# Optimization experiments

Measured on AMD Instinct MI355X. Metric: run time of the kernel, lower is better.

Reference implementation:

```python
import jax, jax.numpy as jnp
import numpy as np
import math

HIDDEN = 768
HEADS = 12
HEAD_DIM = HIDDEN // HEADS
B, N = 128, 196
POS = 196


def setup_inputs() -> dict:
    key = jax.random.key(0)
    ks = jax.random.split(key, 12)
    s = 1.0 / math.sqrt(HIDDEN)
    inp = {
        "x": jax.random.normal(ks[0], (B, N, HIDDEN), dtype=jnp.float32),
        "Wq": jax.random.normal(ks[1], (HIDDEN, HIDDEN), dtype=jnp.float32) * s,
        "bq": jnp.zeros((HIDDEN,), dtype=jnp.float32),
        "Wk": jax.random.normal(ks[2], (HIDDEN, HIDDEN), dtype=jnp.float32) * s,
        "bk": jnp.zeros((HIDDEN,), dtype=jnp.float32),
        "Wv": jax.random.normal(ks[3], (HIDDEN, HIDDEN), dtype=jnp.float32) * s,
        "bv": jnp.zeros((HIDDEN,), dtype=jnp.float32),
        "Wp": jax.random.normal(ks[4], (HIDDEN, HIDDEN), dtype=jnp.float32) * s,
        "bp": jnp.zeros((HIDDEN,), dtype=jnp.float32),
        "pos_bias": jax.random.normal(ks[5], (POS, POS), dtype=jnp.float32) * 0.02,
        "mask": jnp.ones((B, 1, 1, N), dtype=jnp.int32),
    }
    return inp


def reference(x, Wq, bq, Wk, bk, Wv, bv, Wp, bp, pos_bias, mask):
    Bx, Nx, C = x.shape
    H, D = HEADS, HEAD_DIM
    # nn.Linear: y = x @ W.T + b
    q = (x @ Wq.T + bq).reshape(Bx, Nx, H, D).transpose(0, 2, 1, 3)  # [B,H,N,D]
    k = (x @ Wk.T + bk).reshape(Bx, Nx, H, D).transpose(0, 2, 1, 3)
    v = (x @ Wv.T + bv).reshape(Bx, Nx, H, D).transpose(0, 2, 1, 3)
    attn = jnp.einsum('bhnd,bhmd->bhnm', q, k) / math.sqrt(D)
    attn = attn + pos_bias[:Nx, :Nx][None, None, :, :]
    attn = jnp.where(mask == 0, -jnp.inf, attn)
    attn = jax.nn.softmax(attn, axis=-1)
    out = jnp.einsum('bhnm,bhmd->bhnd', attn, v)
    out = out.transpose(0, 2, 1, 3).reshape(Bx, Nx, C)
    return out @ Wp.T + bp
```

## Files before the change

### kernel.cpp

```cpp
#include <hip/hip_runtime.h>
#include <hip/hip_bf16.h>

#define HIDDEN 768
#define HEADS 12
#define HEAD_DIM 64
#define BATCH 128
#define SEQ 196
#define M_TOT (BATCH * SEQ)
#define QKV_N (3 * HIDDEN)

typedef __attribute__((ext_vector_type(8))) short bf16x8;
typedef __attribute__((ext_vector_type(8))) unsigned short u16x8;
typedef __attribute__((ext_vector_type(4))) float f32x4;

__device__ __forceinline__ unsigned short f2bf(float f) {
    unsigned int u = __builtin_bit_cast(unsigned int, f);
    unsigned int r = (u + 0x7fffu + ((u >> 16) & 1u)) >> 16;
    return (unsigned short)r;
}

__device__ __forceinline__ ushort4 cvt4(float4 v) {
    ushort4 o;
    o.x = f2bf(v.x); o.y = f2bf(v.y); o.z = f2bf(v.z); o.w = f2bf(v.w);
    return o;
}

__global__ __launch_bounds__(256) void prep_kernel(
    const float* __restrict__ x,
    const float* __restrict__ Wq, const float* __restrict__ Wk,
    const float* __restrict__ Wv, const float* __restrict__ Wp,
    const float* __restrict__ bq, const float* __restrict__ bk,
    const float* __restrict__ bv,
    unsigned short* __restrict__ xb, unsigned short* __restrict__ wqkv,
    unsigned short* __restrict__ wpb, float* __restrict__ biasq)
{
    const long long NX = (long long)M_TOT * HIDDEN / 4;
    const long long NQ = NX + (long long)QKV_N * HIDDEN / 4;
    const long long NP = NQ + (long long)HIDDEN * HIDDEN / 4;
    const long long NB = NP + QKV_N / 4;
    long long tid = (long long)blockIdx.x * 256 + threadIdx.x;
    if (tid < NX) {
        float4 v = ((const float4*)x)[tid];
        ((ushort4*)xb)[tid] = cvt4(v);
    } else if (tid < NQ) {
        int i = (int)(tid - NX);
        int e = i * 4;
        int row = e / HIDDEN, col = e % HIDDEN;
        const float* s = (row < HIDDEN) ? (Wq + (size_t)row * HIDDEN + col)
                       : (row < 2 * HIDDEN) ? (Wk + (size_t)(row - HIDDEN) * HIDDEN + col)
                       : (Wv + (size_t)(row - 2 * HIDDEN) * HIDDEN + col);
        ((ushort4*)wqkv)[i] = cvt4(*(const float4*)s);
    } else if (tid < NP) {
        int i = (int)(tid - NQ);
        ((ushort4*)wpb)[i] = cvt4(((const float4*)Wp)[i]);
    } else if (tid < NB) {
        int i = (int)(tid - NP);
        int e = i * 4;
        const float* s = (e < HIDDEN) ? (bq + e)
                       : (e < 2 * HIDDEN) ? (bk + (e - HIDDEN))
                       : (bv + (e - 2 * HIDDEN));
        *(float4*)(biasq + e) = *(const float4*)s;
    }
}

template <bool OUT_BF16>
__global__ __launch_bounds__(512, 2) void gemm256(
    const unsigned short* __restrict__ A,
    const unsigned short* __restrict__ B,
    const float* __restrict__ bias,
    void* __restrict__ C, const int Ncols)
{
    __shared__ __align__(16) unsigned short SMEM[65536];
    const int t = threadIdx.x, w = t >> 6, lane = t & 63;
    const int quad = lane >> 4, l15 = lane & 15;
    const int wm = w >> 2, wn = w & 3;

    const int gx = gridDim.x;
    const int nwg = gx * (int)gridDim.y;
    const int orig = blockIdx.y * gx + blockIdx.x;
    const int qq = nwg >> 3, rr = nwg & 7;
    const int xcd = orig & 7, loc = orig >> 3;
    const int wg = (xcd < rr ? xcd * (qq + 1) : rr * (qq + 1) + (xcd - rr) * qq) + loc;
    const int m0 = (wg / gx) * 256, n0 = (wg % gx) * 256;

    const int row64 = t >> 3, slot = t & 7;
    const int ksw = (slot ^ (row64 & 7)) << 3;
    const unsigned short* Ag = A + (size_t)m0 * HIDDEN + ksw;
    const unsigned short* Bg = B + (size_t)n0 * HIDDEN + ksw;
    const int ldsw = (w << 3) * 64;

#define STAGEA(bb, tt, pp)                                                          \
    __builtin_amdgcn_global_load_lds(                                               \
        (__attribute__((address_space(1))) void*)(Ag + (size_t)((pp) * 64 + row64) * HIDDEN + (tt) * 64), \
        (__attribute__((address_space(3))) void*)(SMEM + (bb) * 16384 + (pp) * 4096 + ldsw), 16, 0, 0)
#define STAGEB(bb, tt, pp)                                                          \
    __builtin_amdgcn_global_load_lds(                                               \
        (__attribute__((address_space(1))) void*)(Bg + (size_t)((pp) * 64 + row64) * HIDDEN + (tt) * 64), \
        (__attribute__((address_space(3))) void*)(SMEM + 32768 + (bb) * 16384 + (pp) * 4096 + ldsw), 16, 0, 0)

    const int sw = l15 & 7;
    const int s0 = (quad ^ sw) << 3;
    const int s1 = ((quad + 4) ^ sw) << 3;
    const unsigned short* pa = SMEM + (wm * 128 + l15) * 64;
    const unsigned short* pb = SMEM + 32768 + (wn * 64 + l15) * 64;

    f32x4 acc[8][4] = {};

#pragma unroll
    for (int p = 0; p < 4; ++p) STAGEA(0, 0, p);
#pragma unroll
    for (int p = 0; p < 4; ++p) STAGEB(0, 0, p);
#pragma unroll
    for (int p = 0; p < 4; ++p) STAGEB(1, 1, p);
    asm volatile("s_waitcnt vmcnt(4)" ::: "memory");
    __builtin_amdgcn_s_barrier();

#pragma unroll 2
    for (int kt = 0; kt < 12; ++kt) {
        const int b = kt & 1;
        const unsigned short* pab = pa + b * 16384;
        const unsigned short* pbb = pb + b * 16384;
        bf16x8 Bf[4][2];
        bf16x8 Af[2][2];

#pragma unroll
        for (int ph = 0; ph < 4; ++ph) {
            const int ib = ph * 2;
            if (ph == 0) {
#pragma unroll
                for (int j = 0; j < 4; ++j) {
                    Bf[j][0] = *(const bf16x8*)(pbb + j * 1024 + s0);
                    Bf[j][1] = *(const bf16x8*)(pbb + j * 1024 + s1);
                }
            }
            Af[0][0] = *(const bf16x8*)(pab + ib * 1024 + s0);
            Af[0][1] = *(const bf16x8*)(pab + ib * 1024 + s1);
            Af[1][0] = *(const bf16x8*)(pab + ib * 1024 + 1024 + s0);
            Af[1][1] = *(const bf16x8*)(pab + ib * 1024 + 1024 + s1);
            if (ph == 0 && kt < 11) { STAGEA(b ^ 1, kt + 1, 0); STAGEA(b ^ 1, kt + 1, 1); }
            if (ph == 1 && kt < 11) { STAGEA(b ^ 1, kt + 1, 2); STAGEA(b ^ 1, kt + 1, 3); }
            if (ph == 2 && kt < 10) { STAGEB(b, kt + 2, 0); STAGEB(b, kt + 2, 1); }
            if (ph == 3 && kt < 10) { STAGEB(b, kt + 2, 2); STAGEB(b, kt + 2, 3); }
            __builtin_amdgcn_s_barrier();
            asm volatile("s_waitcnt lgkmcnt(0)" ::: "memory");
            __builtin_amdgcn_sched_barrier(0);
            __builtin_amdgcn_s_setprio(1);
#pragma unroll
            for (int i = 0; i < 2; ++i)
#pragma unroll
                for (int j = 0; j < 4; ++j) {
                    acc[ib + i][j] = __builtin_amdgcn_mfma_f32_16x16x32_bf16(
                        Af[i][0], Bf[j][0], acc[ib + i][j], 0, 0, 0);
                    acc[ib + i][j] = __builtin_amdgcn_mfma_f32_16x16x32_bf16(
                        Af[i][1], Bf[j][1], acc[ib + i][j], 0, 0, 0);
                }
            __builtin_amdgcn_s_setprio(0);
            if (ph == 3) {
                if (kt < 10) { asm volatile("s_waitcnt vmcnt(4)" ::: "memory"); }
                else if (kt == 10) { asm volatile("s_waitcnt vmcnt(0)" ::: "memory"); }
            }
            __builtin_amdgcn_s_barrier();
        }
    }
#undef STAGEA
#undef STAGEB

    __syncthreads();
    float* Cs = (float*)SMEM + w * (16 * 68);
    float bvj[4];
#pragma unroll
    for (int j = 0; j < 4; ++j) bvj[j] = bias[n0 + wn * 64 + j * 16 + l15];

#pragma unroll
    for (int i = 0; i < 8; ++i) {
        __builtin_amdgcn_sched_barrier(0);
#pragma unroll
        for (int j = 0; j < 4; ++j)
#pragma unroll
            for (int r = 0; r < 4; ++r)
                Cs[(quad * 4 + r) * 68 + j * 16 + l15] = acc[i][j][r] + bvj[j];
        __builtin_amdgcn_sched_barrier(0);
        asm volatile("s_waitcnt lgkmcnt(0)" ::: "memory");
        if constexpr (OUT_BF16) {
#pragma unroll
            for (int p = 0; p < 2; ++p) {
                const int row = p * 8 + (lane >> 3);
                const int c0 = (lane & 7) * 8;
                float4 a = *(const float4*)&Cs[row * 68 + c0];
                float4 bb = *(const float4*)&Cs[row * 68 + c0 + 4];
                u16x8 pk;
                pk[0] = f2bf(a.x); pk[1] = f2bf(a.y); pk[2] = f2bf(a.z); pk[3] = f2bf(a.w);
                pk[4] = f2bf(bb.x); pk[5] = f2bf(bb.y); pk[6] = f2bf(bb.z); pk[7] = f2bf(bb.w);
                *(u16x8*)((unsigned short*)C +
                          (size_t)(m0 + wm * 128 + i * 16 + row) * Ncols + n0 + wn * 64 + c0) = pk;
            }
        } else {
#pragma unroll
            for (int p = 0; p < 4; ++p) {
                const int row = p * 4 + (lane >> 4);
                const int c0 = (lane & 15) * 4;
                float4 a = *(const float4*)&Cs[row * 68 + c0];
                *(float4*)((float*)C +
                           (size_t)(m0 + wm * 128 + i * 16 + row) * Ncols + n0 + wn * 64 + c0) = a;
            }
        }
        __builtin_amdgcn_sched_barrier(0);
    }
}

__global__ __launch_bounds__(256, 2) void attn_kernel(
    const unsigned short* __restrict__ QKV,
    const float* __restrict__ pos_bias,
    const int* __restrict__ mask,
    unsigned short* __restrict__ ctx)
{
    __shared__ __align__(16) unsigned short Ks[208 * 72];
    __shared__ __align__(16) unsigned short Vt[64 * 256];
    __shared__ __align__(16) unsigned short Os[4][16 * 72];
    const int b = blockIdx.x / HEADS, h = blockIdx.x % HEADS;
    const int t = threadIdx.x, w = t >> 6, lane = t & 63;
    const int quad = lane >> 4, l15 = lane & 15;
    const size_t base = (size_t)b * SEQ * QKV_N + h * HEAD_DIM;

    for (int c = t; c < SEQ * 8; c += 256) {
        int row = c >> 3, d0 = (c & 7) * 8;
        *(bf16x8*)(Ks + row * 72 + d0) =
            *(const bf16x8*)(QKV + base + (size_t)row * QKV_N + HIDDEN + d0);
    }
    {
        bf16x8 z = {};
        for (int i = t; i < 12 * 9; i += 256) {
            int row = 196 + i / 9, d0 = (i % 9) * 8;
            *(bf16x8*)(Ks + row * 72 + d0) = z;
        }
    }
    for (int i = t; i < 64 * 60; i += 256) {
        int row = i / 60, key = 196 + i % 60;
        int s = (row & 7) ^ ((row >> 3) & 7);
        Vt[row * 256 + ((((key >> 3) ^ s) << 3) | (key & 7))] = 0;
    }
    for (int c = t; c < SEQ * 8; c += 256) {
        int key = c >> 3, d0 = (c & 7) * 8;
        bf16x8 vv = *(const bf16x8*)(QKV + base + (size_t)key * QKV_N + 2 * HIDDEN + d0);
        int cb = key >> 3, kk = key & 7;
#pragma unroll
        for (int j = 0; j < 8; ++j) {
            int row = d0 + j;
            int s = (row & 7) ^ ((row >> 3) & 7);
            Vt[row * 256 + (((cb ^ s) << 3) | kk)] = (unsigned short)vv[j];
        }
    }
    __syncthreads();

    int vs[4];
#pragma unroll
    for (int nt = 0; nt < 4; ++nt) {
        int rr = nt * 16 + l15;
        vs[nt] = (rr & 7) ^ ((rr >> 3) & 7);
    }

    for (int t16 = w; t16 < 13; t16 += 4) {
        const int qrow = min(t16 * 16 + l15, SEQ - 1);
        const unsigned short* qp = QKV + base + (size_t)qrow * QKV_N + quad * 8;
        bf16x8 qf0 = *(const bf16x8*)(qp);
        bf16x8 qf1 = *(const bf16x8*)(qp + 32);

        f32x4 accT[13];
#pragma unroll
        for (int jt = 0; jt < 13; ++jt) {
            const unsigned short* kp = Ks + (jt * 16 + l15) * 72 + quad * 8;
            bf16x8 kf0 = *(const bf16x8*)(kp);
            bf16x8 kf1 = *(const bf16x8*)(kp + 32);
            f32x4 z = {};
            z = __builtin_amdgcn_mfma_f32_16x16x32_bf16(kf0, qf0, z, 0, 0, 0);
            z = __builtin_amdgcn_mfma_f32_16x16x32_bf16(kf1, qf1, z, 0, 0, 0);
            accT[jt] = z;
        }

        float mx = -3e38f;
#pragma unroll
        for (int jt = 0; jt < 13; ++jt) {
            const int key0 = jt * 16 + quad * 4;
            const int kb = min(key0, SEQ - 4);
            float4 pb = *(const float4*)(pos_bias + (size_t)qrow * SEQ + kb);
            int4 mk = *(const int4*)(mask + b * SEQ + kb);
#pragma unroll
            for (int r = 0; r < 4; ++r) {
                const int key = key0 + r;
                const bool cv = (key < SEQ) && ((&mk.x)[r] != 0);
                float v = cv ? (accT[jt][r] * 0.125f + (&pb.x)[r]) : -1e30f;
                accT[jt][r] = v;
                mx = fmaxf(mx, v);
            }
        }
        mx = fmaxf(mx, __shfl_xor(mx, 16, 64));
        mx = fmaxf(mx, __shfl_xor(mx, 32, 64));
        float sm = 0.f;
#pragma unroll
        for (int jt = 0; jt < 13; ++jt)
#pragma unroll
            for (int r = 0; r < 4; ++r) {
                float e = __expf(accT[jt][r] - mx);
                accT[jt][r] = e;
                sm += e;
            }
        sm += __shfl_xor(sm, 16, 64);
        sm += __shfl_xor(sm, 32, 64);
        const float inv = 1.0f / sm;

        unsigned int pk[14][2];
#pragma unroll
        for (int jt = 0; jt < 13; ++jt)
#pragma unroll
            for (int pp = 0; pp < 2; ++pp) {
                unsigned int lo = f2bf(accT[jt][2 * pp] * inv);
                unsigned int hi = f2bf(accT[jt][2 * pp + 1] * inv);
                pk[jt][pp] = (hi << 16) | lo;
            }
        pk[13][0] = 0; pk[13][1] = 0;

        f32x4 o[4] = {};
        const int hi_half = quad >> 1;
        const int sq0 = (quad & 1) * 2 * 16 + l15;
        const int sq1 = sq0 + 16;
#pragma unroll
        for (int kt = 0; kt < 7; ++kt) {
            union { unsigned int u[4]; bf16x8 v; } pf;
#pragma unroll
            for (int u = 0; u < 4; ++u) {
                const int src = (u < 2) ? sq0 : sq1;
                unsigned int a0 = (unsigned int)__shfl((int)pk[2 * kt][u & 1], src, 64);
                unsigned int a1 = (unsigned int)__shfl((int)pk[2 * kt + 1][u & 1], src, 64);
                pf.u[u] = hi_half ? a1 : a0;
            }
#pragma unroll
            for (int nt = 0; nt < 4; ++nt) {
                const int rr = nt * 16 + l15;
                const bf16x8 vf = *(const bf16x8*)(
                    &Vt[rr * 256 + (((kt * 4 + quad) ^ vs[nt]) << 3)]);
                o[nt] = __builtin_amdgcn_mfma_f32_16x16x32_bf16(pf.v, vf, o[nt], 0, 0, 0);
            }
        }

        __builtin_amdgcn_sched_barrier(0);
#pragma unroll
        for (int nt = 0; nt < 4; ++nt)
#pragma unroll
            for (int r = 0; r < 4; ++r)
                Os[w][(quad * 4 + r) * 72 + nt * 16 + l15] = f2bf(o[nt][r]);
        __builtin_amdgcn_sched_barrier(0);
        asm volatile("s_waitcnt lgkmcnt(0)" ::: "memory");
#pragma unroll
        for (int p = 0; p < 2; ++p) {
            const int row = p * 8 + (lane >> 3);
            const int grow = t16 * 16 + row;
            const int c0 = (lane & 7) * 8;
            bf16x8 ov = *(const bf16x8*)&Os[w][row * 72 + c0];
            if (grow < SEQ)
                *(bf16x8*)(ctx + ((size_t)b * SEQ + grow) * HIDDEN + h * HEAD_DIM + c0) = ov;
        }
        __builtin_amdgcn_sched_barrier(0);
    }
}

extern "C" void kernel_launch(void* const* d_in, const int* in_sizes, int n_in,
                              void* d_out, int out_size, void* d_ws, size_t ws_size,
                              hipStream_t stream) {
    const float* x    = (const float*)d_in[0];
    const float* Wq   = (const float*)d_in[1];
    const float* bq   = (const float*)d_in[2];
    const float* Wk   = (const float*)d_in[3];
    const float* bk   = (const float*)d_in[4];
    const float* Wv   = (const float*)d_in[5];
    const float* bv   = (const float*)d_in[6];
    const float* Wp   = (const float*)d_in[7];
    const float* bp   = (const float*)d_in[8];
    const float* pos  = (const float*)d_in[9];
    const int*   mask = (const int*)d_in[10];

    char* ws = (char*)d_ws;
    size_t off = 0;
    auto alloc = [&](size_t bytes) -> char* {
        char* p = ws + off;
        off += (bytes + 255) & ~(size_t)255;
        return p;
    };
    unsigned short* xb    = (unsigned short*)alloc((size_t)M_TOT * HIDDEN * 2);
    unsigned short* wqkv  = (unsigned short*)alloc((size_t)QKV_N * HIDDEN * 2);
    unsigned short* wpb   = (unsigned short*)alloc((size_t)HIDDEN * HIDDEN * 2);
    float*          biasq = (float*)alloc((size_t)QKV_N * 4);
    unsigned short* qkv   = (unsigned short*)alloc((size_t)M_TOT * QKV_N * 2);
    unsigned short* ctx   = (unsigned short*)alloc((size_t)M_TOT * HIDDEN * 2);

    prep_kernel<<<21123, 256, 0, stream>>>(x, Wq, Wk, Wv, Wp, bq, bk, bv,
                                           xb, wqkv, wpb, biasq);
    gemm256<true><<<dim3(QKV_N / 256, M_TOT / 256), 512, 0, stream>>>(
        xb, wqkv, biasq, (void*)qkv, QKV_N);
    attn_kernel<<<BATCH * HEADS, 256, 0, stream>>>(qkv, pos, mask, ctx);
    gemm256<false><<<dim3(HIDDEN / 256, M_TOT / 256), 512, 0, stream>>>(
        ctx, wpb, bp, d_out, HIDDEN);
}
```

Before: 377.2 us.

## Load B fragments directly from global into registers and quad-buffer A in LDS

The GEMM stops staging B tiles through LDS. Each wave now loads its B fragments straight from global memory into registers, one k-tile ahead, while A is staged in a 4-deep LDS ring with prefetch distance two. The workgroup-to-tile mapping becomes column-major so consecutive workgroups share the same B columns, which should improve L2 reuse. This removes LDS traffic and barriers for B and halves the per-phase barriers, but makes B loads uncached per-wave global reads and leaves MFMAs exposed to global latency if the prefetch is not deep enough.

```diff
diff --git a/kernel.cpp b/kernel.cpp
--- a/kernel.cpp
+++ b/kernel.cpp
@@ -75,95 +75,91 @@
     const int quad = lane >> 4, l15 = lane & 15;
     const int wm = w >> 2, wn = w & 3;
 
-    const int gx = gridDim.x;
-    const int nwg = gx * (int)gridDim.y;
-    const int orig = blockIdx.y * gx + blockIdx.x;
-    const int qq = nwg >> 3, rr = nwg & 7;
+    const int gy = gridDim.y;
+    const int nwg = gridDim.x * gy;
+    const int orig = blockIdx.y * gridDim.x + blockIdx.x;
+    const int qq = nwg >> 3, rr2 = nwg & 7;
     const int xcd = orig & 7, loc = orig >> 3;
-    const int wg = (xcd < rr ? xcd * (qq + 1) : rr * (qq + 1) + (xcd - rr) * qq) + loc;
-    const int m0 = (wg / gx) * 256, n0 = (wg % gx) * 256;
+    const int pos = (xcd < rr2 ? xcd * (qq + 1) : rr2 * (qq + 1) + (xcd - rr2) * qq) + loc;
+    const int m0 = (pos % gy) * 256;
+    const int n0 = (pos / gy) * 256;
 
     const int row64 = t >> 3, slot = t & 7;
     const int ksw = (slot ^ (row64 & 7)) << 3;
     const unsigned short* Ag = A + (size_t)m0 * HIDDEN + ksw;
-    const unsigned short* Bg = B + (size_t)n0 * HIDDEN + ksw;
     const int ldsw = (w << 3) * 64;
 
 #define STAGEA(bb, tt, pp)                                                          \
     __builtin_amdgcn_global_load_lds(                                               \
         (__attribute__((address_space(1))) void*)(Ag + (size_t)((pp) * 64 + row64) * HIDDEN + (tt) * 64), \
         (__attribute__((address_space(3))) void*)(SMEM + (bb) * 16384 + (pp) * 4096 + ldsw), 16, 0, 0)
-#define STAGEB(bb, tt, pp)                                                          \
-    __builtin_amdgcn_global_load_lds(                                               \
-        (__attribute__((address_space(1))) void*)(Bg + (size_t)((pp) * 64 + row64) * HIDDEN + (tt) * 64), \
-        (__attribute__((address_space(3))) void*)(SMEM + 32768 + (bb) * 16384 + (pp) * 4096 + ldsw), 16, 0, 0)
 
     const int sw = l15 & 7;
     const int s0 = (quad ^ sw) << 3;
     const int s1 = ((quad + 4) ^ sw) << 3;
     const unsigned short* pa = SMEM + (wm * 128 + l15) * 64;
-    const unsigned short* pb = SMEM + 32768 + (wn * 64 + l15) * 64;
+
+    const unsigned short* Bgf = B + (size_t)(n0 + wn * 64 + l15) * HIDDEN + quad * 8;
 
     f32x4 acc[8][4] = {};
+    bf16x8 Bf[4][2];
 
 #pragma unroll
     for (int p = 0; p < 4; ++p) STAGEA(0, 0, p);
-#pragma unroll
-    for (int p = 0; p < 4; ++p) STAGEB(0, 0, p);
-#pragma unroll
-    for (int p = 0; p < 4; ++p) STAGEB(1, 1, p);
-    asm volatile("s_waitcnt vmcnt(4)" ::: "memory");
+    __builtin_amdgcn_sched_barrier(0);
+#pragma unroll
+    for (int j = 0; j < 4; ++j) {
+        Bf[j][0] = *(const bf16x8*)(Bgf + j * 12288);
+        Bf[j][1] = *(const bf16x8*)(Bgf + j * 12288 + 32);
+    }
+    __builtin_amdgcn_sched_barrier(0);
+#pragma unroll
+    for (int p = 0; p < 4; ++p) STAGEA(1, 1, p);
+    asm volatile("s_waitcnt vmcnt(12)" ::: "memory");
     __builtin_amdgcn_s_barrier();
-
-#pragma unroll 2
+    __builtin_amdgcn_sched_barrier(0);
+
+#pragma unroll
     for (int kt = 0; kt < 12; ++kt) {
-        const int b = kt & 1;
-        const unsigned short* pab = pa + b * 16384;
-        const unsigned short* pbb = pb + b * 16384;
-        bf16x8 Bf[4][2];
-        bf16x8 Af[2][2];
+        const unsigned short* pab = pa + (kt & 3) * 16384;
 
 #pragma unroll
         for (int ph = 0; ph < 4; ++ph) {
             const int ib = ph * 2;
-            if (ph == 0) {
-#pragma unroll
-                for (int j = 0; j < 4; ++j) {
-                    Bf[j][0] = *(const bf16x8*)(pbb + j * 1024 + s0);
-                    Bf[j][1] = *(const bf16x8*)(pbb + j * 1024 + s1);
-                }
-            }
+            bf16x8 Af[2][2];
             Af[0][0] = *(const bf16x8*)(pab + ib * 1024 + s0);
             Af[0][1] = *(const bf16x8*)(pab + ib * 1024 + s1);
             Af[1][0] = *(const bf16x8*)(pab + ib * 1024 + 1024 + s0);
             Af[1][1] = *(const bf16x8*)(pab + ib * 1024 + 1024 + s1);
-            if (ph == 0 && kt < 11) { STAGEA(b ^ 1, kt + 1, 0); STAGEA(b ^ 1, kt + 1, 1); }
-            if (ph == 1 && kt < 11) { STAGEA(b ^ 1, kt + 1, 2); STAGEA(b ^ 1, kt + 1, 3); }
-            if (ph == 2 && kt < 10) { STAGEB(b, kt + 2, 0); STAGEB(b, kt + 2, 1); }
-            if (ph == 3 && kt < 10) { STAGEB(b, kt + 2, 2); STAGEB(b, kt + 2, 3); }
-            __builtin_amdgcn_s_barrier();
-            asm volatile("s_waitcnt lgkmcnt(0)" ::: "memory");
-            __builtin_amdgcn_sched_barrier(0);
-            __builtin_amdgcn_s_setprio(1);
-#pragma unroll
-            for (int i = 0; i < 2; ++i)
-#pragma unroll
-                for (int j = 0; j < 4; ++j) {
+#pragma unroll
+            for (int j = 0; j < 4; ++j)
+#pragma unroll
+                for (int i = 0; i < 2; ++i) {
                     acc[ib + i][j] = __builtin_amdgcn_mfma_f32_16x16x32_bf16(
                         Af[i][0], Bf[j][0], acc[ib + i][j], 0, 0, 0);
                     acc[ib + i][j] = __builtin_amdgcn_mfma_f32_16x16x32_bf16(
                         Af[i][1], Bf[j][1], acc[ib + i][j], 0, 0, 0);
                 }
-            __builtin_amdgcn_s_setprio(0);
-            if (ph == 3) {
-                if (kt < 10) { asm volatile("s_waitcnt vmcnt(4)" ::: "memory"); }
-                else if (kt == 10) { asm volatile("s_waitcnt vmcnt(0)" ::: "memory"); }
-            }
+        }
+
+        if (kt < 11) {
+#pragma unroll
+            for (int j = 0; j < 4; ++j) {
+                Bf[j][0] = *(const bf16x8*)(Bgf + j * 12288 + (kt + 1) * 64);
+                Bf[j][1] = *(const bf16x8*)(Bgf + j * 12288 + (kt + 1) * 64 + 32);
+            }
+            __builtin_amdgcn_sched_barrier(0);
+            if (kt < 10) {
+#pragma unroll
+                for (int p = 0; p < 4; ++p) STAGEA((kt + 2) & 3, kt + 2, p);
+            }
+            if (kt < 10) { asm volatile("s_waitcnt vmcnt(12)" ::: "memory"); }
+            else         { asm volatile("s_waitcnt vmcnt(8)"  ::: "memory"); }
             __builtin_amdgcn_s_barrier();
+            __builtin_amdgcn_sched_barrier(0);
         }
     }
 #undef STAGEA
-#undef STAGEB
 
     __syncthreads();
     float* Cs = (float*)SMEM + w * (16 * 68);
```

Measured after the change: 417.8 us. 1.11x slower.
